# Kernel optimization log

Hardware: AMD Instinct MI355X
Metric: run time of the kernel (lower is better)

The kernel has to match this reference:

```python
import jax, jax.numpy as jnp
import numpy as np

B, S, D, HD, P = 4, 8192, 1024, 128, 32
EPS_LN = 1e-5

def setup_inputs() -> dict:
    key = jax.random.key(0)
    ks = jax.random.split(key, 12)
    x      = jax.random.normal(ks[0], (B, S, D), dtype=jnp.float32)
    W_proj = jax.random.normal(ks[1], (8, D, HD), dtype=jnp.float32) * 0.02
    freqs  = jax.random.normal(ks[2], (8, HD), dtype=jnp.float32) * 0.01
    W_pol  = jax.random.normal(ks[3], (8, HD, P), dtype=jnp.float32) * 0.05
    b_pol  = jnp.zeros((8, P), jnp.float32)
    W_imp1 = jax.random.normal(ks[4], (1, 16), dtype=jnp.float32) * 0.5
    b_imp1 = jnp.zeros((16,), jnp.float32)
    W_imp2 = jax.random.normal(ks[5], (16, 1), dtype=jnp.float32) * 0.5
    b_imp2 = jnp.zeros((1,), jnp.float32)
    W_out  = jax.random.normal(ks[6], (D, D), dtype=jnp.float32) * 0.02
    b_out  = jnp.zeros((D,), jnp.float32)
    gamma  = jnp.ones((D,), jnp.float32)
    beta   = jnp.zeros((D,), jnp.float32)
    return dict(x=x, W_proj=W_proj, freqs=freqs, W_pol=W_pol, b_pol=b_pol,
                W_imp1=W_imp1, b_imp1=b_imp1, W_imp2=W_imp2, b_imp2=b_imp2,
                W_out=W_out, b_out=b_out, gamma=gamma, beta=beta)

def reference(x, W_proj, freqs, W_pol, b_pol, W_imp1, b_imp1, W_imp2, b_imp2,
              W_out, b_out, gamma, beta):
    # heads[i] = (x @ W_proj[i]) * cos(pi * freqs[i])   -> (8, B, S, HD)
    heads = jnp.einsum('bsd,hde->hbse', x, W_proj) * jnp.cos(freqs * jnp.pi)[:, None, None, :]

    # --- GuaXiangDuiChong: impedance matrix (B, 8, 8) ---
    hm = heads.mean(axis=2)                                   # (8, B, HD)
    pv = jnp.tanh(jnp.einsum('hbd,hdp->bhp', hm, W_pol) + b_pol[None])  # (B, 8, P)
    pm = pv / jnp.maximum(jnp.linalg.norm(pv, axis=-1, keepdims=True), 1e-12)
    dp = jnp.einsum('bhp,bgp->bhg', pm, pm)                   # (B, 8, 8)
    z = jax.nn.gelu(dp[..., None] * W_imp1[0] + b_imp1, approximate=False)  # (B,8,8,16)
    imp = jax.nn.softplus(jnp.einsum('bhgk,ko->bhgo', z, W_imp2)[..., 0] + b_imp2[0])
    imp = imp * (1.0 - jnp.eye(8, dtype=imp.dtype))           # zero diagonal

    # --- head mixing. Causal masked-mean collapses to row scale (s+1)/S ---
    coeff = (0.1 / (1.0 + imp)) * (1.0 - jnp.eye(8, dtype=imp.dtype))  # (B,8,8), j!=i
    mix = jnp.einsum('big,gbsd->ibsd', coeff, heads)          # (8, B, S, HD)
    causal_scale = (jnp.arange(S, dtype=x.dtype) + 1.0) / S   # (S,)
    out_heads = heads + causal_scale[None, None, :, None] * mix

    merged = out_heads.transpose(1, 2, 0, 3).reshape(B, S, D)
    proj = jnp.einsum('bsd,de->bse', merged, W_out) + b_out   # dropout = identity (eval)
    y = proj + x
    mu = y.mean(axis=-1, keepdims=True)
    var = y.var(axis=-1, keepdims=True)
    y = (y - mu) * jax.lax.rsqrt(var + EPS_LN) * gamma + beta
    return y, imp
```

## Files before the change

### kernel.cpp

```cpp
#include <hip/hip_runtime.h>
#include <hip/hip_bf16.h>
#include <math.h>

typedef __bf16 bf16;
typedef __bf16 bf16x2 __attribute__((ext_vector_type(2)));
typedef __bf16 bf16x4 __attribute__((ext_vector_type(4)));
typedef __bf16 bf16x8 __attribute__((ext_vector_type(8)));
typedef float  f32x4  __attribute__((ext_vector_type(4)));

#define NB 4
#define SS 8192
#define DD 1024
#define MM 32768
#define KK 1024
#define NN 1024
#define PI_F 3.14159265358979323846f

__device__ __forceinline__ void gl2lds16(const bf16* g, bf16* l) {
    __builtin_amdgcn_global_load_lds(
        (const __attribute__((address_space(1))) void*)g,
        (__attribute__((address_space(3))) void*)l, 16, 0, 0);
}

__global__ __launch_bounds__(256) void prep_all(const float* __restrict__ x,
                                                bf16* __restrict__ xb,
                                                const float* __restrict__ W_proj,
                                                const float* __restrict__ freqs,
                                                const float* __restrict__ W_out,
                                                bf16* __restrict__ WbT1,
                                                bf16* __restrict__ WoT,
                                                float* __restrict__ hm) {
    int blk = blockIdx.x;
    if (blk < MM / 2) {
        size_t i = (size_t)blk * 2048 + threadIdx.x * 8;
        float4 v0 = *(const float4*)&x[i];
        float4 v1 = *(const float4*)&x[i + 4];
        bf16x8 o;
        o[0] = (bf16)v0.x; o[1] = (bf16)v0.y; o[2] = (bf16)v0.z; o[3] = (bf16)v0.w;
        o[4] = (bf16)v1.x; o[5] = (bf16)v1.y; o[6] = (bf16)v1.z; o[7] = (bf16)v1.w;
        *(bf16x8*)&xb[i] = o;
    } else {
        int idx = (blk - MM / 2) * 256 + threadIdx.x;
        int n = idx >> 10, k = idx & 1023;
        int h = n >> 7, d = n & 127;
        float c = cosf(PI_F * freqs[n]);
        WbT1[idx] = (bf16)(W_proj[(size_t)h * (DD * 128) + (size_t)k * 128 + d] * c);
        WoT[idx]  = (bf16)(W_out[(size_t)k * DD + n]);
        if (idx < NB * DD) hm[idx] = 0.0f;
    }
}

#define FENCE  asm volatile("" ::: "memory")
#define BARRIER do { FENCE; __builtin_amdgcn_s_barrier(); FENCE; } while (0)
#define PRIO1  __builtin_amdgcn_s_setprio(1)
#define PRIO0  __builtin_amdgcn_s_setprio(0)
#define VMC(N) asm volatile("s_waitcnt vmcnt(" #N ")" ::: "memory")
#define NOPS   ((void)0)

#define STG(g0, g1, uk, ldsBase)                                  \
    gl2lds16((g0) + (uk), &sm[(ldsBase) + w * 512]);              \
    gl2lds16((g1) + (uk), &sm[(ldsBase) + 4096 + w * 512]);

#define READ_A2(MQ, ab)                                                          \
    _Pragma("unroll") for (int m_ = 0; m_ < 4; ++m_) {                           \
        a[m_ * 2 + 0] = *(const bf16x8*)&sm[(ab) + aoff0 + ((MQ)*64 + m_*16)*64];\
        a[m_ * 2 + 1] = *(const bf16x8*)&sm[(ab) + aoff1 + ((MQ)*64 + m_*16)*64];\
    }
#define READ_B2(NQ, bfr, bb)                                                     \
    _Pragma("unroll") for (int n_ = 0; n_ < 2; ++n_) {                           \
        bfr[n_ * 2 + 0] = *(const bf16x8*)&sm[(bb) + boff0 + ((NQ)*32 + n_*16)*64];\
        bfr[n_ * 2 + 1] = *(const bf16x8*)&sm[(bb) + boff1 + ((NQ)*32 + n_*16)*64];\
    }

#define MFMA_Q(MQ, NQ, bfr)                                                    \
    _Pragma("unroll") for (int m_ = 0; m_ < 4; ++m_)                           \
    _Pragma("unroll") for (int n_ = 0; n_ < 2; ++n_)                           \
    _Pragma("unroll") for (int ks_ = 0; ks_ < 2; ++ks_)                        \
        acc[(MQ) * 4 + m_][(NQ) * 2 + n_] =                                    \
            __builtin_amdgcn_mfma_f32_16x16x32_bf16(                           \
                a[m_ * 2 + ks_], bfr[n_ * 2 + ks_],                            \
                acc[(MQ) * 4 + m_][(NQ) * 2 + n_], 0, 0, 0);

#define ITER(uk1, STG3, STG4, STG5, STG6, STG7, STG8, VM4, VM8)                \
  { BARRIER; STG(gA00, gA01, (uk1), 16384);                                    \
    PRIO1; READ_A2(0, 0); READ_B2(0, blo, 32768); MFMA_Q(0, 0, blo); PRIO0;    \
    BARRIER; STG(gA10, gA11, (uk1), 24576);                                    \
    PRIO1; READ_B2(1, bhi, 32768); MFMA_Q(0, 1, bhi); PRIO0;                   \
    BARRIER; STG3;                                                             \
    PRIO1; READ_A2(1, 0); MFMA_Q(1, 1, bhi); PRIO0;                            \
    BARRIER; STG4; VM4;                                                        \
    PRIO1; MFMA_Q(1, 0, blo); PRIO0;                                           \
    BARRIER; STG5;                                                             \
    PRIO1; READ_A2(0, 16384); READ_B2(0, blo, 49152); MFMA_Q(0, 0, blo); PRIO0;\
    BARRIER; STG6;                                                             \
    PRIO1; READ_B2(1, bhi, 49152); MFMA_Q(0, 1, bhi); PRIO0;                   \
    BARRIER; STG7;                                                             \
    PRIO1; READ_A2(1, 16384); MFMA_Q(1, 1, bhi); PRIO0;                        \
    BARRIER; STG8; VM8;                                                        \
    PRIO1; MFMA_Q(1, 0, blo); PRIO0;                                           \
  }

template <int MODE>
__global__ __launch_bounds__(512, 2)
void gemm256(const bf16* __restrict__ A, int lda, const bf16* __restrict__ Bt,
             bf16* __restrict__ Cstr, const bf16* __restrict__ residb,
             const float* __restrict__ bias, float* __restrict__ hm) {
    __shared__ bf16 sm[65536];
    const int tid = threadIdx.x;
    const int lane = tid & 63, w = tid >> 6;
    const int wr = w >> 2, wc = w & 3;
    const int l15 = lane & 15, l4 = lane >> 4;

    int wg = blockIdx.x;
    int swz = (wg & 7) * 64 + (wg >> 3);
    const int mt = swz >> 2, ntile = swz & 3;
    const int row0 = mt * 256, col0 = ntile * 256;

    const int aoff0 = (wr * 128 + l15) * 64 + ((l4 ^ (l15 & 7)) << 3);
    const int aoff1 = aoff0 ^ 32;
    const int boff0 = (wc * 64 + l15) * 64 + ((l4 ^ (l15 & 7)) << 3);
    const int boff1 = boff0 ^ 32;

    const int srow = tid >> 3;
    const int scb  = (tid & 7) ^ (srow & 7);
    const bf16* gA00 = A + (size_t)(row0 + srow) * lda + scb * 8;
    const bf16* gA01 = gA00 + (size_t)64 * lda;
    const bf16* gA10 = gA00 + (size_t)128 * lda;
    const bf16* gA11 = gA00 + (size_t)192 * lda;
    const bf16* gB00 = Bt + (size_t)(col0 + srow) * 1024 + scb * 8;
    const bf16* gB01 = gB00 + 64 * 1024;
    const bf16* gB10 = gB00 + 128 * 1024;
    const bf16* gB11 = gB00 + 192 * 1024;

    f32x4 acc[8][4] = {};
    bf16x8 a[8], blo[4], bhi[4];

    STG(gA00, gA01, 0,  0);     STG(gA10, gA11, 0,  8192);
    STG(gB00, gB01, 0,  32768); STG(gB10, gB11, 0,  40960);
    STG(gA00, gA01, 64, 16384); STG(gA10, gA11, 64, 24576);
    STG(gB00, gB01, 64, 49152); STG(gB10, gB11, 64, 57344);
    VMC(0);

#pragma unroll 1
    for (int i = 0; i < 7; ++i) {
        const int uk1 = (2 * i + 1) * 64;
        const int uk2 = (2 * i + 2) * 64;
        const int uk3 = (2 * i + 3) * 64;
        ITER(uk1,
             STG(gB00, gB01, uk2, 32768), STG(gB10, gB11, uk2, 40960),
             STG(gA00, gA01, uk2, 0),     STG(gA10, gA11, uk2, 8192),
             STG(gB00, gB01, uk3, 49152), STG(gB10, gB11, uk3, 57344),
             VMC(4), VMC(4));
    }
    ITER(960, NOPS, NOPS, NOPS, NOPS, NOPS, NOPS, VMC(0), NOPS);

    if (MODE == 0) {
        const int batch = row0 >> 13;
#pragma unroll
        for (int mg = 0; mg < 8; ++mg) {
            int rbase = row0 + wr * 128 + (mg >> 2) * 64 + (mg & 3) * 16 + l4 * 4;
#pragma unroll
            for (int j = 0; j < 4; ++j) {
                size_t row = rbase + j;
#pragma unroll
                for (int ng = 0; ng < 4; ++ng) {
                    int col = col0 + wc * 64 + ng * 16 + l15;
                    Cstr[row * 2048 + col] = (bf16)acc[mg][ng][j];
                }
            }
        }
#pragma unroll
        for (int ng = 0; ng < 4; ++ng) {
            float s = 0;
#pragma unroll
            for (int mg = 0; mg < 8; ++mg)
#pragma unroll
                for (int j = 0; j < 4; ++j) s += acc[mg][ng][j];
            int col = col0 + wc * 64 + ng * 16 + l15;
            atomicAdd(&hm[batch * DD + col], s);
        }
    } else {
        float bi[4];
#pragma unroll
        for (int ng = 0; ng < 4; ++ng) bi[ng] = bias[col0 + wc * 64 + ng * 16 + l15];
#pragma unroll
        for (int mg = 0; mg < 8; ++mg) {
            int rbase = row0 + wr * 128 + (mg >> 2) * 64 + (mg & 3) * 16 + l4 * 4;
#pragma unroll
            for (int j = 0; j < 4; ++j) {
                size_t row = rbase + j;
#pragma unroll
                for (int ng = 0; ng < 4; ++ng) {
                    int col = col0 + wc * 64 + ng * 16 + l15;
                    Cstr[row * 2048 + col] =
                        (bf16)(acc[mg][ng][j] + bi[ng] + (float)residb[row * 1024 + col]);
                }
            }
        }
    }
}

__global__ __launch_bounds__(256) void imp_pm(const float* __restrict__ hm,
                                              const float* __restrict__ W_pol,
                                              const float* __restrict__ b_pol,
                                              float* __restrict__ pm) {
    int bh = blockIdx.x;
    int b = bh >> 3, h = bh & 7;
    int tid = threadIdx.x;
    int p = tid & 31, dg = tid >> 5;
    float partial = 0;
#pragma unroll
    for (int dd = 0; dd < 16; ++dd) {
        int d = dg * 16 + dd;
        partial += hm[b * DD + h * 128 + d] * (1.0f / SS)
                 * W_pol[(h * 128 + d) * 32 + p];
    }
    __shared__ float red[8][32];
    red[dg][p] = partial;
    __syncthreads();
    if (tid < 32) {
        float a = b_pol[h * 32 + p];
#pragma unroll
        for (int g = 0; g < 8; ++g) a += red[g][p];
        float pv = tanhf(a);
        float ss = pv * pv;
#pragma unroll
        for (int off = 16; off > 0; off >>= 1) ss += __shfl_xor(ss, off);
        pm[bh * 32 + p] = pv / fmaxf(sqrtf(ss), 1e-12f);
    }
}

__global__ __launch_bounds__(256) void imp_mlp(const float* __restrict__ pm,
                                               const float* __restrict__ W_imp1,
                                               const float* __restrict__ b_imp1,
                                               const float* __restrict__ W_imp2,
                                               const float* __restrict__ b_imp2,
                                               float* __restrict__ imp_out,
                                               float* __restrict__ coeff) {
    __shared__ float pms[32][32];
    int tid = threadIdx.x;
    for (int i = tid; i < 1024; i += 256) pms[i >> 5][i & 31] = pm[i];
    __syncthreads();
    int b2 = tid >> 6, h2 = (tid >> 3) & 7, g = tid & 7;
    float dp = 0;
#pragma unroll
    for (int q = 0; q < 32; ++q) dp += pms[b2 * 8 + h2][q] * pms[b2 * 8 + g][q];
    float a2 = 0;
#pragma unroll
    for (int kk = 0; kk < 16; ++kk) {
        float zin = dp * W_imp1[kk] + b_imp1[kk];
        float zg = 0.5f * zin * (1.0f + erff(zin * 0.70710678118654752f));
        a2 += zg * W_imp2[kk];
    }
    float spin = a2 + b_imp2[0];
    float impv = (spin > 20.0f) ? spin : log1pf(expf(spin));
    if (h2 == g) impv = 0.0f;
    imp_out[tid] = impv;
    coeff[tid] = (h2 == g) ? 0.0f : 0.1f / (1.0f + impv);
}

__global__ __launch_bounds__(256) void mix_k(const char* __restrict__ slots,
                                             const float* __restrict__ coeff,
                                             char* __restrict__ slots_w) {
    __shared__ float cf[64];
    int tid = threadIdx.x;
    size_t r0 = (size_t)blockIdx.x * 16;
    int b = (int)(r0 >> 13);
    if (tid < 64) cf[tid] = coeff[b * 64 + tid];
    __syncthreads();
    size_t r = r0 + (tid >> 4);
    int dd = tid & 15;
    int s = (int)(r & (SS - 1));
    float cs = (float)(s + 1) * (1.0f / SS);
    const bf16* hrow = (const bf16*)(slots + r * 4096);
    bf16* mrow = (bf16*)(slots_w + r * 4096 + 2048);
    float v[8][8];
#pragma unroll
    for (int g = 0; g < 8; ++g) {
        bf16x8 t8 = *(const bf16x8*)&hrow[g * 128 + dd * 8];
#pragma unroll
        for (int e = 0; e < 8; ++e) v[g][e] = (float)t8[e];
    }
#pragma unroll
    for (int h = 0; h < 8; ++h) {
        bf16x8 o;
#pragma unroll
        for (int e = 0; e < 8; ++e) {
            float acc = 0;
#pragma unroll
            for (int g = 0; g < 8; ++g) acc += cf[h * 8 + g] * v[g][e];
            o[e] = (bf16)(v[h][e] + cs * acc);
        }
        *(bf16x8*)&mrow[h * 128 + dd * 8] = o;
    }
}

__global__ __launch_bounds__(256) void ln_k(char* __restrict__ slots,
                                            const float* __restrict__ gamma,
                                            const float* __restrict__ beta) {
    int tid = threadIdx.x;
    size_t r = (size_t)blockIdx.x * 2 + (tid >> 7);
    int t = tid & 127;
    const bf16* zrow = (const bf16*)(slots + r * 4096);
    float* yrow = (float*)(slots + r * 4096);
    int e0 = t * 8;
    bf16x8 zv = *(const bf16x8*)&zrow[e0];
    float v[8];
    float sum = 0, sq = 0;
#pragma unroll
    for (int e = 0; e < 8; ++e) {
        v[e] = (float)zv[e];
        sum += v[e];
        sq  += v[e] * v[e];
    }
#pragma unroll
    for (int off = 32; off > 0; off >>= 1) {
        sum += __shfl_down(sum, off);
        sq  += __shfl_down(sq, off);
    }
    __shared__ float red[4][2];
    int lane = tid & 63, wv = tid >> 6;
    if (lane == 0) { red[wv][0] = sum; red[wv][1] = sq; }
    __syncthreads();
    int rw = (tid >> 7) * 2;
    float tot = red[rw][0] + red[rw + 1][0];
    float tsq = red[rw][1] + red[rw + 1][1];
    float mu  = tot * (1.0f / DD);
    float var = tsq * (1.0f / DD) - mu * mu;
    float rs  = rsqrtf(var + 1e-5f);
    float4 g0 = *(const float4*)&gamma[e0];
    float4 g1 = *(const float4*)&gamma[e0 + 4];
    float4 b0 = *(const float4*)&beta[e0];
    float4 b1 = *(const float4*)&beta[e0 + 4];
    float4 o0, o1;
    o0.x = (v[0] - mu) * rs * g0.x + b0.x;
    o0.y = (v[1] - mu) * rs * g0.y + b0.y;
    o0.z = (v[2] - mu) * rs * g0.z + b0.z;
    o0.w = (v[3] - mu) * rs * g0.w + b0.w;
    o1.x = (v[4] - mu) * rs * g1.x + b1.x;
    o1.y = (v[5] - mu) * rs * g1.y + b1.y;
    o1.z = (v[6] - mu) * rs * g1.z + b1.z;
    o1.w = (v[7] - mu) * rs * g1.w + b1.w;
    *(float4*)&yrow[e0] = o0;
    *(float4*)&yrow[e0 + 4] = o1;
}

extern "C" void kernel_launch(void* const* d_in, const int* in_sizes, int n_in,
                              void* d_out, int out_size, void* d_ws, size_t ws_size,
                              hipStream_t stream) {
    const float* x      = (const float*)d_in[0];
    const float* W_proj = (const float*)d_in[1];
    const float* freqs  = (const float*)d_in[2];
    const float* W_pol  = (const float*)d_in[3];
    const float* b_pol  = (const float*)d_in[4];
    const float* W_imp1 = (const float*)d_in[5];
    const float* b_imp1 = (const float*)d_in[6];
    const float* W_imp2 = (const float*)d_in[7];
    const float* b_imp2 = (const float*)d_in[8];
    const float* W_out  = (const float*)d_in[9];
    const float* b_out  = (const float*)d_in[10];
    const float* gamma  = (const float*)d_in[11];
    const float* beta   = (const float*)d_in[12];

    char* ws = (char*)d_ws;
    bf16* xb     = (bf16*)ws;
    bf16* WbT1   = (bf16*)(ws + ((size_t)64 << 20));
    bf16* WoT    = (bf16*)(ws + ((size_t)66 << 20));
    float* hm    = (float*)(ws + ((size_t)68 << 20));
    float* coeff = (float*)(ws + ((size_t)68 << 20) + 16384);
    float* pm    = (float*)(ws + ((size_t)68 << 20) + 20480);

    char* slots = (char*)d_out;
    float* imp_out = (float*)d_out + (size_t)MM * DD;

    prep_all<<<MM / 2 + 4096, 256, 0, stream>>>(x, xb, W_proj, freqs, W_out,
                                                WbT1, WoT, hm);

    gemm256<0><<<512, 512, 0, stream>>>(xb, 1024, WbT1, (bf16*)slots,
                                        nullptr, nullptr, hm);

    imp_pm<<<32, 256, 0, stream>>>(hm, W_pol, b_pol, pm);
    imp_mlp<<<1, 256, 0, stream>>>(pm, W_imp1, b_imp1, W_imp2, b_imp2,
                                   imp_out, coeff);

    mix_k<<<MM / 16, 256, 0, stream>>>(slots, coeff, slots);

    gemm256<1><<<512, 512, 0, stream>>>((const bf16*)slots + 1024, 2048, WoT,
                                        (bf16*)slots, xb, b_out, nullptr);

    ln_k<<<MM / 2, 256, 0, stream>>>(slots, gamma, beta);
}
```

Before: 264.4 us.

## Fuse fp32-to-bf16 conversion of x into first GEMM's A-tile loading

Drops the separate pass that converts x to a bf16 copy. The first GEMM now loads fp32 x directly into registers, converts to bf16 and writes the swizzled tile into LDS, staged across the pipeline. The second GEMM reads the fp32 residual x instead of the bf16 copy. This removes a 128MB read plus 64MB write pass. In exchange the A path moves from direct global-to-LDS loads to register staging with more VGPR pressure, and the GEMM reads twice as many bytes for A.

```diff
diff --git a/kernel.cpp b/kernel.cpp
--- a/kernel.cpp
+++ b/kernel.cpp
@@ -22,32 +22,19 @@
         (__attribute__((address_space(3))) void*)l, 16, 0, 0);
 }
 
-__global__ __launch_bounds__(256) void prep_all(const float* __restrict__ x,
-                                                bf16* __restrict__ xb,
-                                                const float* __restrict__ W_proj,
-                                                const float* __restrict__ freqs,
-                                                const float* __restrict__ W_out,
-                                                bf16* __restrict__ WbT1,
-                                                bf16* __restrict__ WoT,
-                                                float* __restrict__ hm) {
-    int blk = blockIdx.x;
-    if (blk < MM / 2) {
-        size_t i = (size_t)blk * 2048 + threadIdx.x * 8;
-        float4 v0 = *(const float4*)&x[i];
-        float4 v1 = *(const float4*)&x[i + 4];
-        bf16x8 o;
-        o[0] = (bf16)v0.x; o[1] = (bf16)v0.y; o[2] = (bf16)v0.z; o[3] = (bf16)v0.w;
-        o[4] = (bf16)v1.x; o[5] = (bf16)v1.y; o[6] = (bf16)v1.z; o[7] = (bf16)v1.w;
-        *(bf16x8*)&xb[i] = o;
-    } else {
-        int idx = (blk - MM / 2) * 256 + threadIdx.x;
-        int n = idx >> 10, k = idx & 1023;
-        int h = n >> 7, d = n & 127;
-        float c = cosf(PI_F * freqs[n]);
-        WbT1[idx] = (bf16)(W_proj[(size_t)h * (DD * 128) + (size_t)k * 128 + d] * c);
-        WoT[idx]  = (bf16)(W_out[(size_t)k * DD + n]);
-        if (idx < NB * DD) hm[idx] = 0.0f;
-    }
+__global__ __launch_bounds__(256) void prep_w(const float* __restrict__ W_proj,
+                                              const float* __restrict__ freqs,
+                                              const float* __restrict__ W_out,
+                                              bf16* __restrict__ WbT1,
+                                              bf16* __restrict__ WoT,
+                                              float* __restrict__ hm) {
+    int idx = blockIdx.x * 256 + threadIdx.x;
+    int n = idx >> 10, k = idx & 1023;
+    int h = n >> 7, d = n & 127;
+    float c = cosf(PI_F * freqs[n]);
+    WbT1[idx] = (bf16)(W_proj[(size_t)h * (DD * 128) + (size_t)k * 128 + d] * c);
+    WoT[idx]  = (bf16)(W_out[(size_t)k * DD + n]);
+    if (idx < NB * DD) hm[idx] = 0.0f;
 }
 
 #define FENCE  asm volatile("" ::: "memory")
@@ -55,6 +42,7 @@
 #define PRIO1  __builtin_amdgcn_s_setprio(1)
 #define PRIO0  __builtin_amdgcn_s_setprio(0)
 #define VMC(N) asm volatile("s_waitcnt vmcnt(" #N ")" ::: "memory")
+#define LGKM0  asm volatile("s_waitcnt lgkmcnt(0)" ::: "memory")
 #define NOPS   ((void)0)
 
 #define STG(g0, g1, uk, ldsBase)                                  \
@@ -81,7 +69,130 @@
                 a[m_ * 2 + ks_], bfr[n_ * 2 + ks_],                            \
                 acc[(MQ) * 4 + m_][(NQ) * 2 + n_], 0, 0, 0);
 
-#define ITER(uk1, STG3, STG4, STG5, STG6, STG7, STG8, VM4, VM8)                \
+#define ISSA(uk)                                                               \
+    areg[0] = *(const f32x4*)(gAh0 + (uk));                                    \
+    areg[1] = *(const f32x4*)(gAh0 + (uk) + 4);                                \
+    areg[2] = *(const f32x4*)(gAh0 + (uk) + 8);                                \
+    areg[3] = *(const f32x4*)(gAh0 + (uk) + 12);                               \
+    areg[4] = *(const f32x4*)(gAh1 + (uk));                                    \
+    areg[5] = *(const f32x4*)(gAh1 + (uk) + 4);                                \
+    areg[6] = *(const f32x4*)(gAh1 + (uk) + 8);                                \
+    areg[7] = *(const f32x4*)(gAh1 + (uk) + 12);
+
+#define CVT1(dst, lo, hi)                                                      \
+    { bf16x8 w_; w_[0]=(bf16)(lo).x; w_[1]=(bf16)(lo).y; w_[2]=(bf16)(lo).z;   \
+      w_[3]=(bf16)(lo).w; w_[4]=(bf16)(hi).x; w_[5]=(bf16)(hi).y;              \
+      w_[6]=(bf16)(hi).z; w_[7]=(bf16)(hi).w; *(bf16x8*)(dst) = w_; }
+
+#define WRA(ab)                                                                \
+    CVT1(&sm[(ab) + wA0],        areg[0], areg[1]);                            \
+    CVT1(&sm[(ab) + wA1],        areg[2], areg[3]);                            \
+    CVT1(&sm[(ab) + 8192 + wA0], areg[4], areg[5]);                            \
+    CVT1(&sm[(ab) + 8192 + wA1], areg[6], areg[7]);
+
+#define ITER_G1(uk1, STG3, STG4, STG7, STG8, ISS5, VM4, VM8, WR8)              \
+  { BARRIER; ISSA(uk1);                                                        \
+    PRIO1; READ_A2(0, 0); READ_B2(0, blo, 32768); MFMA_Q(0, 0, blo); PRIO0;    \
+    BARRIER;                                                                   \
+    PRIO1; READ_B2(1, bhi, 32768); MFMA_Q(0, 1, bhi); PRIO0;                   \
+    BARRIER; STG3;                                                             \
+    PRIO1; READ_A2(1, 0); MFMA_Q(1, 1, bhi); PRIO0;                            \
+    BARRIER; STG4; VM4; WRA(16384);                                            \
+    PRIO1; MFMA_Q(1, 0, blo); PRIO0; LGKM0;                                    \
+    BARRIER; ISS5;                                                             \
+    PRIO1; READ_A2(0, 16384); READ_B2(0, blo, 49152); MFMA_Q(0, 0, blo); PRIO0;\
+    BARRIER;                                                                   \
+    PRIO1; READ_B2(1, bhi, 49152); MFMA_Q(0, 1, bhi); PRIO0;                   \
+    BARRIER; STG7;                                                             \
+    PRIO1; READ_A2(1, 16384); MFMA_Q(1, 1, bhi); PRIO0;                        \
+    BARRIER; STG8; VM8; WR8;                                                   \
+    PRIO1; MFMA_Q(1, 0, blo); PRIO0; LGKM0;                                    \
+  }
+
+__global__ __launch_bounds__(512, 2)
+void gemm_g1(const float* __restrict__ X, const bf16* __restrict__ Bt,
+             bf16* __restrict__ Cstr, float* __restrict__ hm) {
+    __shared__ bf16 sm[65536];
+    const int tid = threadIdx.x;
+    const int lane = tid & 63, w = tid >> 6;
+    const int wr = w >> 2, wc = w & 3;
+    const int l15 = lane & 15, l4 = lane >> 4;
+
+    int wg = blockIdx.x;
+    int swz = (wg & 7) * 64 + (wg >> 3);
+    const int mt = swz >> 2, ntile = swz & 3;
+    const int row0 = mt * 256, col0 = ntile * 256;
+
+    const int aoff0 = (wr * 128 + l15) * 64 + ((l4 ^ (l15 & 7)) << 3);
+    const int aoff1 = aoff0 ^ 32;
+    const int boff0 = (wc * 64 + l15) * 64 + ((l4 ^ (l15 & 7)) << 3);
+    const int boff1 = boff0 ^ 32;
+
+    const int rA = tid >> 2;
+    const int c0 = (tid & 3) * 2;
+    const float* gAh0 = X + (size_t)(row0 + rA) * 1024 + c0 * 8;
+    const float* gAh1 = gAh0 + (size_t)128 * 1024;
+    const int wA0 = rA * 64 + ((c0 ^ (rA & 7)) << 3);
+    const int wA1 = rA * 64 + (((c0 + 1) ^ (rA & 7)) << 3);
+
+    const int srow = tid >> 3;
+    const int scb  = (tid & 7) ^ (srow & 7);
+    const bf16* gB00 = Bt + (size_t)(col0 + srow) * 1024 + scb * 8;
+    const bf16* gB01 = gB00 + 64 * 1024;
+    const bf16* gB10 = gB00 + 128 * 1024;
+    const bf16* gB11 = gB00 + 192 * 1024;
+
+    f32x4 acc[8][4] = {};
+    bf16x8 a[8], blo[4], bhi[4];
+    f32x4 areg[8];
+
+    ISSA(0);
+    STG(gB00, gB01, 0,  32768); STG(gB10, gB11, 0,  40960);
+    STG(gB00, gB01, 64, 49152); STG(gB10, gB11, 64, 57344);
+    VMC(8);
+    WRA(0);
+    VMC(4);
+    LGKM0;
+
+#pragma unroll 1
+    for (int i = 0; i < 7; ++i) {
+        const int uk1 = (2 * i + 1) * 64;
+        const int uk2 = (2 * i + 2) * 64;
+        const int uk3 = (2 * i + 3) * 64;
+        ITER_G1(uk1,
+                STG(gB00, gB01, uk2, 32768), STG(gB10, gB11, uk2, 40960),
+                STG(gB00, gB01, uk3, 49152), STG(gB10, gB11, uk3, 57344),
+                ISSA(uk2), VMC(4), VMC(4), WRA(0));
+    }
+    ITER_G1(960, NOPS, NOPS, NOPS, NOPS, NOPS, VMC(0), VMC(0), NOPS);
+
+    const int batch = row0 >> 13;
+#pragma unroll
+    for (int mg = 0; mg < 8; ++mg) {
+        int rbase = row0 + wr * 128 + (mg >> 2) * 64 + (mg & 3) * 16 + l4 * 4;
+#pragma unroll
+        for (int j = 0; j < 4; ++j) {
+            size_t row = rbase + j;
+#pragma unroll
+            for (int ng = 0; ng < 4; ++ng) {
+                int col = col0 + wc * 64 + ng * 16 + l15;
+                Cstr[row * 2048 + col] = (bf16)acc[mg][ng][j];
+            }
+        }
+    }
+#pragma unroll
+    for (int ng = 0; ng < 4; ++ng) {
+        float s = 0;
+#pragma unroll
+        for (int mg = 0; mg < 8; ++mg)
+#pragma unroll
+            for (int j = 0; j < 4; ++j) s += acc[mg][ng][j];
+        int col = col0 + wc * 64 + ng * 16 + l15;
+        atomicAdd(&hm[batch * DD + col], s);
+    }
+}
+
+#define ITER2(uk1, STG3, STG4, STG5, STG6, STG7, STG8, VM4, VM8)               \
   { BARRIER; STG(gA00, gA01, (uk1), 16384);                                    \
     PRIO1; READ_A2(0, 0); READ_B2(0, blo, 32768); MFMA_Q(0, 0, blo); PRIO0;    \
     BARRIER; STG(gA10, gA11, (uk1), 24576);                                    \
@@ -100,11 +211,10 @@
     PRIO1; MFMA_Q(1, 0, blo); PRIO0;                                           \
   }
 
-template <int MODE>
 __global__ __launch_bounds__(512, 2)
-void gemm256(const bf16* __restrict__ A, int lda, const bf16* __restrict__ Bt,
-             bf16* __restrict__ Cstr, const bf16* __restrict__ residb,
-             const float* __restrict__ bias, float* __restrict__ hm) {
+void gemm_g2(const bf16* __restrict__ A, const bf16* __restrict__ Bt,
+             bf16* __restrict__ Cstr, const float* __restrict__ resid,
+             const float* __restrict__ bias) {
     __shared__ bf16 sm[65536];
     const int tid = threadIdx.x;
     const int lane = tid & 63, w = tid >> 6;
@@ -123,6 +233,7 @@
 
     const int srow = tid >> 3;
     const int scb  = (tid & 7) ^ (srow & 7);
+    const int lda = 2048;
     const bf16* gA00 = A + (size_t)(row0 + srow) * lda + scb * 8;
     const bf16* gA01 = gA00 + (size_t)64 * lda;
     const bf16* gA10 = gA00 + (size_t)128 * lda;
@@ -146,55 +257,28 @@
         const int uk1 = (2 * i + 1) * 64;
         const int uk2 = (2 * i + 2) * 64;
         const int uk3 = (2 * i + 3) * 64;
-        ITER(uk1,
-             STG(gB00, gB01, uk2, 32768), STG(gB10, gB11, uk2, 40960),
-             STG(gA00, gA01, uk2, 0),     STG(gA10, gA11, uk2, 8192),
-             STG(gB00, gB01, uk3, 49152), STG(gB10, gB11, uk3, 57344),
-             VMC(4), VMC(4));
-    }
-    ITER(960, NOPS, NOPS, NOPS, NOPS, NOPS, NOPS, VMC(0), NOPS);
-
-    if (MODE == 0) {
-        const int batch = row0 >> 13;
-#pragma unroll
-        for (int mg = 0; mg < 8; ++mg) {
-            int rbase = row0 + wr * 128 + (mg >> 2) * 64 + (mg & 3) * 16 + l4 * 4;
-#pragma unroll
-            for (int j = 0; j < 4; ++j) {
-                size_t row = rbase + j;
-#pragma unroll
-                for (int ng = 0; ng < 4; ++ng) {
-                    int col = col0 + wc * 64 + ng * 16 + l15;
-                    Cstr[row * 2048 + col] = (bf16)acc[mg][ng][j];
-                }
-            }
-        }
-#pragma unroll
-        for (int ng = 0; ng < 4; ++ng) {
-            float s = 0;
-#pragma unroll
-            for (int mg = 0; mg < 8; ++mg)
-#pragma unroll
-                for (int j = 0; j < 4; ++j) s += acc[mg][ng][j];
-            int col = col0 + wc * 64 + ng * 16 + l15;
-            atomicAdd(&hm[batch * DD + col], s);
-        }
-    } else {
-        float bi[4];
-#pragma unroll
-        for (int ng = 0; ng < 4; ++ng) bi[ng] = bias[col0 + wc * 64 + ng * 16 + l15];
-#pragma unroll
-        for (int mg = 0; mg < 8; ++mg) {
-            int rbase = row0 + wr * 128 + (mg >> 2) * 64 + (mg & 3) * 16 + l4 * 4;
-#pragma unroll
-            for (int j = 0; j < 4; ++j) {
-                size_t row = rbase + j;
-#pragma unroll
-                for (int ng = 0; ng < 4; ++ng) {
-                    int col = col0 + wc * 64 + ng * 16 + l15;
-                    Cstr[row * 2048 + col] =
-                        (bf16)(acc[mg][ng][j] + bi[ng] + (float)residb[row * 1024 + col]);
-                }
+        ITER2(uk1,
+              STG(gB00, gB01, uk2, 32768), STG(gB10, gB11, uk2, 40960),
+              STG(gA00, gA01, uk2, 0),     STG(gA10, gA11, uk2, 8192),
+              STG(gB00, gB01, uk3, 49152), STG(gB10, gB11, uk3, 57344),
+              VMC(4), VMC(4));
+    }
+    ITER2(960, NOPS, NOPS, NOPS, NOPS, NOPS, NOPS, VMC(0), NOPS);
+
+    float bi[4];
+#pragma unroll
+    for (int ng = 0; ng < 4; ++ng) bi[ng] = bias[col0 + wc * 64 + ng * 16 + l15];
+#pragma unroll
+    for (int mg = 0; mg < 8; ++mg) {
+        int rbase = row0 + wr * 128 + (mg >> 2) * 64 + (mg & 3) * 16 + l4 * 4;
+#pragma unroll
+        for (int j = 0; j < 4; ++j) {
+            size_t row = rbase + j;
+#pragma unroll
+            for (int ng = 0; ng < 4; ++ng) {
+                int col = col0 + wc * 64 + ng * 16 + l15;
+                Cstr[row * 2048 + col] =
+                    (bf16)(acc[mg][ng][j] + bi[ng] + resid[row * 1024 + col]);
             }
         }
     }
@@ -363,21 +447,18 @@
     const float* beta   = (const float*)d_in[12];
 
     char* ws = (char*)d_ws;
-    bf16* xb     = (bf16*)ws;
-    bf16* WbT1   = (bf16*)(ws + ((size_t)64 << 20));
-    bf16* WoT    = (bf16*)(ws + ((size_t)66 << 20));
-    float* hm    = (float*)(ws + ((size_t)68 << 20));
-    float* coeff = (float*)(ws + ((size_t)68 << 20) + 16384);
-    float* pm    = (float*)(ws + ((size_t)68 << 20) + 20480);
+    bf16* WbT1   = (bf16*)ws;
+    bf16* WoT    = (bf16*)(ws + ((size_t)2 << 20));
+    float* hm    = (float*)(ws + ((size_t)4 << 20));
+    float* coeff = (float*)(ws + ((size_t)4 << 20) + 16384);
+    float* pm    = (float*)(ws + ((size_t)4 << 20) + 20480);
 
     char* slots = (char*)d_out;
     float* imp_out = (float*)d_out + (size_t)MM * DD;
 
-    prep_all<<<MM / 2 + 4096, 256, 0, stream>>>(x, xb, W_proj, freqs, W_out,
-                                                WbT1, WoT, hm);
-
-    gemm256<0><<<512, 512, 0, stream>>>(xb, 1024, WbT1, (bf16*)slots,
-                                        nullptr, nullptr, hm);
+    prep_w<<<4096, 256, 0, stream>>>(W_proj, freqs, W_out, WbT1, WoT, hm);
+
+    gemm_g1<<<512, 512, 0, stream>>>(x, WbT1, (bf16*)slots, hm);
 
     imp_pm<<<32, 256, 0, stream>>>(hm, W_pol, b_pol, pm);
     imp_mlp<<<1, 256, 0, stream>>>(pm, W_imp1, b_imp1, W_imp2, b_imp2,
@@ -385,8 +466,8 @@
 
     mix_k<<<MM / 16, 256, 0, stream>>>(slots, coeff, slots);
 
-    gemm256<1><<<512, 512, 0, stream>>>((const bf16*)slots + 1024, 2048, WoT,
-                                        (bf16*)slots, xb, b_out, nullptr);
+    gemm_g2<<<512, 512, 0, stream>>>((const bf16*)slots + 1024, WoT,
+                                     (bf16*)slots, x, b_out);
 
     ln_k<<<MM / 2, 256, 0, stream>>>(slots, gamma, beta);
 }
```

Result: slower. 276.7 us (+4.7%).
